# Kernel optimization log

Measured on AMD Instinct MI355X. Metric: run time of the kernel, lower is better.

## Reference

```python
import jax, jax.numpy as jnp
import numpy as np

EMBED_DIM = 512
NUM_HEADS = 8
HEAD_DIM = EMBED_DIM // NUM_HEADS


def setup_inputs() -> dict:
    key = jax.random.key(0)
    k1, k2, kw, kb, kow, kob = jax.random.split(key, 6)
    B, L, C = 2, 2048, EMBED_DIM
    s = 1.0 / np.sqrt(C)
    return {
        "x1": jax.random.normal(k1, (B, L, C), dtype=jnp.float32),
        "x2": jax.random.normal(k2, (B, L, C), dtype=jnp.float32),
        # nn.Linear(embed_dim, 3*embed_dim): weight [3C, C], bias [3C]
        "qkv_w": jax.random.uniform(kw, (3 * C, C), jnp.float32, -s, s),
        "qkv_b": jax.random.uniform(kb, (3 * C,), jnp.float32, -s, s),
        # nn.Linear(embed_dim, embed_dim): weight [C, C], bias [C]
        "out_w": jax.random.uniform(kow, (C, C), jnp.float32, -s, s),
        "out_b": jax.random.uniform(kob, (C,), jnp.float32, -s, s),
    }


def _qkv(x, qkv_w, qkv_b):
    B, L, C = x.shape
    H, D = NUM_HEADS, C // NUM_HEADS
    # Linear: x @ W^T + b, then view(B, L, H, 3, D) and split along the '3' axis
    qkv = (jnp.einsum("blc,fc->blf", x, qkv_w) + qkv_b).reshape(B, L, H, 3, D)
    qkv = jnp.transpose(qkv, (3, 0, 2, 1, 4))  # [3, B, H, L, D]
    return qkv[0], qkv[1], qkv[2]


def _attend(q, k, v):
    # q,k,v: [B, H, L, D]; scale by 1/sqrt(D)
    scale = 1.0 / np.sqrt(q.shape[-1]).astype(np.float32)
    scores = jnp.einsum("bhqd,bhkd->bhqk", q, k) * scale  # [B,H,L,L]
    attn = jax.nn.softmax(scores, axis=-1)
    out = jnp.einsum("bhqk,bhkd->bhqd", attn, v)
    B, H, L, D = out.shape
    return jnp.transpose(out, (0, 2, 1, 3)).reshape(B, L, H * D)


def reference(x1, x2, qkv_w, qkv_b, out_w, out_b):
    q1, k1, v1 = _qkv(x1, qkv_w, qkv_b)
    q2, k2, v2 = _qkv(x2, qkv_w, qkv_b)
    out1 = _attend(q1, k2, v2)  # q from x1, k/v from x2
    out2 = _attend(q2, k1, v1)  # q from x2, k/v from x1
    out1 = jnp.einsum("blc,fc->blf", out1, out_w) + out_b
    out2 = jnp.einsum("blc,fc->blf", out2, out_w) + out_b
    return (out1, out2)
```

## Files before the change

### kernel.cpp

```cpp
#include <hip/hip_runtime.h>
#include <stdint.h>

typedef unsigned short u16;
typedef unsigned int u32;
typedef short bf16x8 __attribute__((ext_vector_type(8)));
typedef float f32x4 __attribute__((ext_vector_type(4)));
typedef float f32x16 __attribute__((ext_vector_type(16)));

#define K_DIM 512

__device__ __forceinline__ u16 f2bf(float f) {
  union { float f; u32 u; } v; v.f = f;
  return (u16)((v.u + 0x8000u) >> 16);
}
__device__ __forceinline__ u32 pk2(float lo, float hi) {
  union { float f; u32 u; } a, b; a.f = lo; b.f = hi;
  return __builtin_amdgcn_perm(b.u + 0x8000u, a.u + 0x8000u, 0x07060302u);
}

__global__ void cvt_kernel(const float* __restrict__ x1, const float* __restrict__ x2,
                           const float* __restrict__ qkvw, const float* __restrict__ outw,
                           u16* __restrict__ xb, u16* __restrict__ wqkv, u16* __restrict__ wout) {
  int tid = blockIdx.x * 256 + threadIdx.x;
  const float4* src; u16* dst; int idx = tid;
  if (idx < 524288)        { src = (const float4*)x1;   dst = xb; }
  else if (idx < 1048576)  { src = (const float4*)x2;   dst = xb + 2097152; idx -= 524288; }
  else if (idx < 1245184)  { src = (const float4*)qkvw; dst = wqkv;         idx -= 1048576; }
  else                     { src = (const float4*)outw; dst = wout;         idx -= 1245184; }
  float4 v = src[idx];
  *(uint2*)&dst[idx * 4] = make_uint2(pk2(v.x, v.y), pk2(v.z, v.w));
}

#define LDA 40

__global__ __launch_bounds__(256, 3) void qkv_gemm(
    const u16* __restrict__ A, const u16* __restrict__ W, const float* __restrict__ bias,
    u16* __restrict__ qb, u16* __restrict__ kb, u16* __restrict__ vtb) {
  __shared__ __align__(16) u16 As[2][128 * LDA];
  __shared__ __align__(16) u16 Bs[2][128 * LDA];
  const int t = threadIdx.x;
  const int m0 = blockIdx.x * 128, n0 = blockIdx.y * 128;
  const int lane = t & 63, l16 = lane & 15, quad = lane >> 4;
  const int w = t >> 6;
  const int wm = (w >> 1) * 64, wn = (w & 1) * 64;
  const int sr = t >> 2, sc = (t & 3) * 8;

  const u16* Ap = A + (size_t)(m0 + sr) * K_DIM + sc;
  const u16* Wp = W + (size_t)(n0 + sr) * K_DIM + sc;

  f32x4 acc[4][4];
#pragma unroll
  for (int i = 0; i < 4; ++i)
#pragma unroll
    for (int j = 0; j < 4; ++j) acc[i][j] = (f32x4){0.f, 0.f, 0.f, 0.f};

  uint4 ra0 = *(const uint4*)(Ap);
  uint4 ra1 = *(const uint4*)(Ap + 64 * K_DIM);
  uint4 rb0 = *(const uint4*)(Wp);
  uint4 rb1 = *(const uint4*)(Wp + 64 * K_DIM);
  *(uint4*)&As[0][sr * LDA + sc] = ra0;
  *(uint4*)&As[0][(sr + 64) * LDA + sc] = ra1;
  *(uint4*)&Bs[0][sr * LDA + sc] = rb0;
  *(uint4*)&Bs[0][(sr + 64) * LDA + sc] = rb1;
  ra0 = *(const uint4*)(Ap + 32);
  ra1 = *(const uint4*)(Ap + 64 * K_DIM + 32);
  rb0 = *(const uint4*)(Wp + 32);
  rb1 = *(const uint4*)(Wp + 64 * K_DIM + 32);
  __syncthreads();

  for (int kt = 0; kt < 16; ++kt) {
    const int cur = kt & 1, nxt = cur ^ 1;
    if (kt < 15) {
      *(uint4*)&As[nxt][sr * LDA + sc] = ra0;
      *(uint4*)&As[nxt][(sr + 64) * LDA + sc] = ra1;
      *(uint4*)&Bs[nxt][sr * LDA + sc] = rb0;
      *(uint4*)&Bs[nxt][(sr + 64) * LDA + sc] = rb1;
    }
    if (kt < 14) {
      int ko = (kt + 2) * 32;
      ra0 = *(const uint4*)(Ap + ko);
      ra1 = *(const uint4*)(Ap + 64 * K_DIM + ko);
      rb0 = *(const uint4*)(Wp + ko);
      rb1 = *(const uint4*)(Wp + 64 * K_DIM + ko);
    }
    bf16x8 af[4], bfr[4];
#pragma unroll
    for (int mi = 0; mi < 4; ++mi)
      af[mi] = *(const bf16x8*)&As[cur][(wm + mi * 16 + l16) * LDA + quad * 8];
#pragma unroll
    for (int ni = 0; ni < 4; ++ni)
      bfr[ni] = *(const bf16x8*)&Bs[cur][(wn + ni * 16 + l16) * LDA + quad * 8];
#pragma unroll
    for (int mi = 0; mi < 4; ++mi)
#pragma unroll
      for (int ni = 0; ni < 4; ++ni)
        acc[mi][ni] = __builtin_amdgcn_mfma_f32_16x16x32_bf16(bfr[ni], af[mi], acc[mi][ni], 0, 0, 0);
    __syncthreads();
  }

  const int fbase = n0 + wn;
  const int h = fbase / 192;
  const int s = (fbase - h * 192) >> 6;
  float4 bv[4];
#pragma unroll
  for (int ni = 0; ni < 4; ++ni)
    bv[ni] = *(const float4*)&bias[fbase + ni * 16 + quad * 4];
  const int bh = m0 >> 11;
  const int lbase = (m0 & 2047) + wm;

  if (s == 2) {
    u16* dst = vtb + (size_t)((bh * 8 + h) * 64) * 2048;
#pragma unroll
    for (int mi = 0; mi < 4; ++mi) {
      int l = lbase + mi * 16 + l16;
#pragma unroll
      for (int ni = 0; ni < 4; ++ni)
#pragma unroll
        for (int r = 0; r < 4; ++r)
          dst[(ni * 16 + quad * 4 + r) * 2048 + l] = f2bf(acc[mi][ni][r] + bv[ni][r]);
    }
  } else {
    u16* dst = (s == 0 ? qb : kb) + (size_t)((bh * 8 + h) * 2048) * 64;
    const float sc2 = (s == 0) ? 0.18033688011112042f : 1.0f;
#pragma unroll
    for (int mi = 0; mi < 4; ++mi) {
      int l = lbase + mi * 16 + l16;
#pragma unroll
      for (int ni = 0; ni < 4; ++ni) {
        float v0 = (acc[mi][ni][0] + bv[ni][0]) * sc2;
        float v1 = (acc[mi][ni][1] + bv[ni][1]) * sc2;
        float v2 = (acc[mi][ni][2] + bv[ni][2]) * sc2;
        float v3 = (acc[mi][ni][3] + bv[ni][3]) * sc2;
        *(uint2*)&dst[(size_t)l * 64 + ni * 16 + quad * 4] = make_uint2(pk2(v0, v1), pk2(v2, v3));
      }
    }
  }
}

#define LQ 72
#define LP 72

__global__ __launch_bounds__(256, 2) void attn_kernel(
    const u16* __restrict__ qb, const u16* __restrict__ kb, const u16* __restrict__ vtb,
    u16* __restrict__ attnb) {
  __shared__ __align__(16) u16 Ks[64 * LQ];
  __shared__ __align__(16) u16 VTs[64 * LQ];
  __shared__ __align__(16) u16 Ps[128 * LP];

  const int t = threadIdx.x;
  const int w = t >> 6, lane = t & 63, l32 = lane & 31, h2 = lane >> 5;
  const int bid = blockIdx.x;
  const int comb = bid & 31;
  const int qt = bid >> 5;
  const int h = comb & 7, bb = (comb >> 3) & 1, pair = comb >> 4;
  const int in_q = pair, in_kv = pair ^ 1;

  const u16* Qg = qb + (size_t)((in_q * 2 + bb) * 8 + h) * 2048 * 64;
  const u16* Kg = kb + (size_t)((in_kv * 2 + bb) * 8 + h) * 2048 * 64;
  const u16* Vg = vtb + (size_t)((in_kv * 2 + bb) * 8 + h) * 64 * 2048;

#pragma unroll
  for (int u = 0; u < 4; ++u) {
    int idx = u * 256 + t;
    int row = idx >> 3, seg = (idx & 7) * 8;
    *(uint4*)&Ps[row * LP + seg] = *(const uint4*)(Qg + (qt * 128 + row) * 64 + seg);
  }
  const int srow = t >> 3, sseg = (t & 7) * 8;
  uint4 rk0 = *(const uint4*)(Kg + srow * 64 + sseg);
  uint4 rk1 = *(const uint4*)(Kg + (srow + 32) * 64 + sseg);
  uint4 rv0 = *(const uint4*)(Vg + srow * 2048 + sseg);
  uint4 rv1 = *(const uint4*)(Vg + (srow + 32) * 2048 + sseg);
  __syncthreads();

  bf16x8 qf[4];
#pragma unroll
  for (int ks = 0; ks < 4; ++ks)
    qf[ks] = *(const bf16x8*)&Ps[(w * 32 + l32) * LP + ks * 16 + h2 * 8];

  f32x16 oacc[2];
#pragma unroll
  for (int mi = 0; mi < 2; ++mi)
#pragma unroll
    for (int r = 0; r < 16; ++r) oacc[mi][r] = 0.f;
  float rs = 0.f;

  u16* Pw = &Ps[w * 32 * LP];

  for (int kt = 0; kt < 32; ++kt) {
    *(uint4*)&Ks[srow * LQ + sseg] = rk0;
    *(uint4*)&Ks[(srow + 32) * LQ + sseg] = rk1;
    *(uint4*)&VTs[srow * LQ + sseg] = rv0;
    *(uint4*)&VTs[(srow + 32) * LQ + sseg] = rv1;
    __syncthreads();
    if (kt < 31) {
      int ko = (kt + 1) * 64;
      rk0 = *(const uint4*)(Kg + (ko + srow) * 64 + sseg);
      rk1 = *(const uint4*)(Kg + (ko + srow + 32) * 64 + sseg);
      rv0 = *(const uint4*)(Vg + srow * 2048 + ko + sseg);
      rv1 = *(const uint4*)(Vg + (srow + 32) * 2048 + ko + sseg);
    }

    f32x16 sacc[2];
#pragma unroll
    for (int mi = 0; mi < 2; ++mi)
#pragma unroll
      for (int r = 0; r < 16; ++r) sacc[mi][r] = 0.f;
#pragma unroll
    for (int ks = 0; ks < 4; ++ks) {
      bf16x8 kfr0 = *(const bf16x8*)&Ks[(l32) * LQ + ks * 16 + h2 * 8];
      bf16x8 kfr1 = *(const bf16x8*)&Ks[(32 + l32) * LQ + ks * 16 + h2 * 8];
      sacc[0] = __builtin_amdgcn_mfma_f32_32x32x16_bf16(kfr0, qf[ks], sacc[0], 0, 0, 0);
      sacc[1] = __builtin_amdgcn_mfma_f32_32x32x16_bf16(kfr1, qf[ks], sacc[1], 0, 0, 0);
    }

#pragma unroll
    for (int mi = 0; mi < 2; ++mi)
#pragma unroll
      for (int rg = 0; rg < 4; ++rg) {
        float p0 = __builtin_amdgcn_exp2f(sacc[mi][rg * 4 + 0]);
        float p1 = __builtin_amdgcn_exp2f(sacc[mi][rg * 4 + 1]);
        float p2 = __builtin_amdgcn_exp2f(sacc[mi][rg * 4 + 2]);
        float p3 = __builtin_amdgcn_exp2f(sacc[mi][rg * 4 + 3]);
        rs += (p0 + p1) + (p2 + p3);
        *(uint2*)&Pw[l32 * LP + mi * 32 + rg * 8 + h2 * 4] = make_uint2(pk2(p0, p1), pk2(p2, p3));
      }

#pragma unroll
    for (int ks = 0; ks < 4; ++ks) {
      bf16x8 pf = *(const bf16x8*)&Pw[l32 * LP + ks * 16 + h2 * 8];
      bf16x8 vf0 = *(const bf16x8*)&VTs[(l32) * LQ + ks * 16 + h2 * 8];
      bf16x8 vf1 = *(const bf16x8*)&VTs[(32 + l32) * LQ + ks * 16 + h2 * 8];
      oacc[0] = __builtin_amdgcn_mfma_f32_32x32x16_bf16(vf0, pf, oacc[0], 0, 0, 0);
      oacc[1] = __builtin_amdgcn_mfma_f32_32x32x16_bf16(vf1, pf, oacc[1], 0, 0, 0);
    }
    __syncthreads();
  }

  rs += __shfl_xor(rs, 32);
  const float inv = 1.0f / rs;
  const int row = in_q * 4096 + bb * 2048 + qt * 128 + w * 32 + l32;
#pragma unroll
  for (int mi = 0; mi < 2; ++mi)
#pragma unroll
    for (int rg = 0; rg < 4; ++rg) {
      float v0 = oacc[mi][rg * 4 + 0] * inv;
      float v1 = oacc[mi][rg * 4 + 1] * inv;
      float v2 = oacc[mi][rg * 4 + 2] * inv;
      float v3 = oacc[mi][rg * 4 + 3] * inv;
      *(uint2*)&attnb[(size_t)row * 512 + h * 64 + mi * 32 + rg * 8 + h2 * 4] =
          make_uint2(pk2(v0, v1), pk2(v2, v3));
    }
}

__global__ __launch_bounds__(256, 2) void out_gemm(
    const u16* __restrict__ A, const u16* __restrict__ W, const float* __restrict__ bias,
    float* __restrict__ out) {
  __shared__ __align__(16) u16 As[2][64 * LDA];
  __shared__ __align__(16) u16 Bs[2][128 * LDA];
  const int t = threadIdx.x;
  const int m0 = blockIdx.x * 64, n0 = blockIdx.y * 128;
  const int lane = t & 63, l16 = lane & 15, quad = lane >> 4;
  const int w = t >> 6;
  const int wm = (w & 1) * 32, wn = (w >> 1) * 64;
  const int ar = t >> 2, ac = (t & 3) * 8;
  const int sr = t >> 2, sc = (t & 3) * 8;

  const u16* Ap = A + (size_t)(m0 + ar) * K_DIM + ac;
  const u16* Wp = W + (size_t)(n0 + sr) * K_DIM + sc;

  f32x4 acc[2][4];
#pragma unroll
  for (int i = 0; i < 2; ++i)
#pragma unroll
    for (int j = 0; j < 4; ++j) acc[i][j] = (f32x4){0.f, 0.f, 0.f, 0.f};

  uint4 ra = *(const uint4*)Ap;
  uint4 rb0 = *(const uint4*)(Wp);
  uint4 rb1 = *(const uint4*)(Wp + 64 * K_DIM);
  *(uint4*)&As[0][ar * LDA + ac] = ra;
  *(uint4*)&Bs[0][sr * LDA + sc] = rb0;
  *(uint4*)&Bs[0][(sr + 64) * LDA + sc] = rb1;
  ra = *(const uint4*)(Ap + 32);
  rb0 = *(const uint4*)(Wp + 32);
  rb1 = *(const uint4*)(Wp + 64 * K_DIM + 32);
  __syncthreads();

  for (int kt = 0; kt < 16; ++kt) {
    const int cur = kt & 1, nxt = cur ^ 1;
    if (kt < 15) {
      *(uint4*)&As[nxt][ar * LDA + ac] = ra;
      *(uint4*)&Bs[nxt][sr * LDA + sc] = rb0;
      *(uint4*)&Bs[nxt][(sr + 64) * LDA + sc] = rb1;
    }
    if (kt < 14) {
      int ko = (kt + 2) * 32;
      ra = *(const uint4*)(Ap + ko);
      rb0 = *(const uint4*)(Wp + ko);
      rb1 = *(const uint4*)(Wp + 64 * K_DIM + ko);
    }
    bf16x8 af[2], bfr[4];
#pragma unroll
    for (int mi = 0; mi < 2; ++mi)
      af[mi] = *(const bf16x8*)&As[cur][(wm + mi * 16 + l16) * LDA + quad * 8];
#pragma unroll
    for (int ni = 0; ni < 4; ++ni)
      bfr[ni] = *(const bf16x8*)&Bs[cur][(wn + ni * 16 + l16) * LDA + quad * 8];
#pragma unroll
    for (int mi = 0; mi < 2; ++mi)
#pragma unroll
      for (int ni = 0; ni < 4; ++ni)
        acc[mi][ni] = __builtin_amdgcn_mfma_f32_16x16x32_bf16(af[mi], bfr[ni], acc[mi][ni], 0, 0, 0);
    __syncthreads();
  }

#pragma unroll
  for (int ni = 0; ni < 4; ++ni) {
    int f = n0 + wn + ni * 16 + l16;
    float bv = bias[f];
#pragma unroll
    for (int mi = 0; mi < 2; ++mi)
#pragma unroll
      for (int r = 0; r < 4; ++r) {
        int m = m0 + wm + mi * 16 + quad * 4 + r;
        out[(size_t)m * 512 + f] = acc[mi][ni][r] + bv;
      }
  }
}

extern "C" void kernel_launch(void* const* d_in, const int* in_sizes, int n_in,
                              void* d_out, int out_size, void* d_ws, size_t ws_size,
                              hipStream_t stream) {
  const float* x1   = (const float*)d_in[0];
  const float* x2   = (const float*)d_in[1];
  const float* qkvw = (const float*)d_in[2];
  const float* qkvb = (const float*)d_in[3];
  const float* outw = (const float*)d_in[4];
  const float* outb = (const float*)d_in[5];
  float* out = (float*)d_out;
  char* ws = (char*)d_ws;

  u16* xb    = (u16*)(ws + 0);
  u16* wqkv  = (u16*)(ws + 8388608);
  u16* wout  = (u16*)(ws + 9961472);
  u16* qb    = (u16*)(ws + 10485760);
  u16* kb    = (u16*)(ws + 18874368);
  u16* vtb   = (u16*)(ws + 27262976);
  u16* attnb = (u16*)(ws + 0);

  cvt_kernel<<<5120, 256, 0, stream>>>(x1, x2, qkvw, outw, xb, wqkv, wout);

  dim3 g1(64, 12);
  qkv_gemm<<<g1, 256, 0, stream>>>(xb, wqkv, qkvb, qb, kb, vtb);

  attn_kernel<<<512, 256, 0, stream>>>(qb, kb, vtb, attnb);

  dim3 g3(128, 4);
  out_gemm<<<g3, 256, 0, stream>>>(attnb, wout, outb, out);
}
```

Measured before the change: 160.5 us.

## Double-buffer K/V tiles and keep P in registers via permlane32 swap

```diff
diff --git a/kernel.cpp b/kernel.cpp
--- a/kernel.cpp
+++ b/kernel.cpp
@@ -138,14 +138,12 @@
 }
 
 #define LQ 72
-#define LP 72
 
 __global__ __launch_bounds__(256, 2) void attn_kernel(
     const u16* __restrict__ qb, const u16* __restrict__ kb, const u16* __restrict__ vtb,
     u16* __restrict__ attnb) {
-  __shared__ __align__(16) u16 Ks[64 * LQ];
-  __shared__ __align__(16) u16 VTs[64 * LQ];
-  __shared__ __align__(16) u16 Ps[128 * LP];
+  __shared__ __align__(16) u16 Ks[2][64 * LQ];
+  __shared__ __align__(16) u16 VTs[2][64 * LQ];
 
   const int t = threadIdx.x;
   const int w = t >> 6, lane = t & 63, l32 = lane & 31, h2 = lane >> 5;
@@ -159,23 +157,26 @@
   const u16* Kg = kb + (size_t)((in_kv * 2 + bb) * 8 + h) * 2048 * 64;
   const u16* Vg = vtb + (size_t)((in_kv * 2 + bb) * 8 + h) * 64 * 2048;
 
-#pragma unroll
-  for (int u = 0; u < 4; ++u) {
-    int idx = u * 256 + t;
-    int row = idx >> 3, seg = (idx & 7) * 8;
-    *(uint4*)&Ps[row * LP + seg] = *(const uint4*)(Qg + (qt * 128 + row) * 64 + seg);
-  }
   const int srow = t >> 3, sseg = (t & 7) * 8;
   uint4 rk0 = *(const uint4*)(Kg + srow * 64 + sseg);
   uint4 rk1 = *(const uint4*)(Kg + (srow + 32) * 64 + sseg);
   uint4 rv0 = *(const uint4*)(Vg + srow * 2048 + sseg);
   uint4 rv1 = *(const uint4*)(Vg + (srow + 32) * 2048 + sseg);
+
+  bf16x8 qf[4];
+#pragma unroll
+  for (int ks = 0; ks < 4; ++ks)
+    qf[ks] = *(const bf16x8*)(Qg + (qt * 128 + w * 32 + l32) * 64 + ks * 16 + h2 * 8);
+
+  *(uint4*)&Ks[0][srow * LQ + sseg] = rk0;
+  *(uint4*)&Ks[0][(srow + 32) * LQ + sseg] = rk1;
+  *(uint4*)&VTs[0][srow * LQ + sseg] = rv0;
+  *(uint4*)&VTs[0][(srow + 32) * LQ + sseg] = rv1;
+  rk0 = *(const uint4*)(Kg + (64 + srow) * 64 + sseg);
+  rk1 = *(const uint4*)(Kg + (64 + srow + 32) * 64 + sseg);
+  rv0 = *(const uint4*)(Vg + srow * 2048 + 64 + sseg);
+  rv1 = *(const uint4*)(Vg + (srow + 32) * 2048 + 64 + sseg);
   __syncthreads();
-
-  bf16x8 qf[4];
-#pragma unroll
-  for (int ks = 0; ks < 4; ++ks)
-    qf[ks] = *(const bf16x8*)&Ps[(w * 32 + l32) * LP + ks * 16 + h2 * 8];
 
   f32x16 oacc[2];
 #pragma unroll
@@ -184,21 +185,9 @@
     for (int r = 0; r < 16; ++r) oacc[mi][r] = 0.f;
   float rs = 0.f;
 
-  u16* Pw = &Ps[w * 32 * LP];
-
+#pragma unroll 2
   for (int kt = 0; kt < 32; ++kt) {
-    *(uint4*)&Ks[srow * LQ + sseg] = rk0;
-    *(uint4*)&Ks[(srow + 32) * LQ + sseg] = rk1;
-    *(uint4*)&VTs[srow * LQ + sseg] = rv0;
-    *(uint4*)&VTs[(srow + 32) * LQ + sseg] = rv1;
-    __syncthreads();
-    if (kt < 31) {
-      int ko = (kt + 1) * 64;
-      rk0 = *(const uint4*)(Kg + (ko + srow) * 64 + sseg);
-      rk1 = *(const uint4*)(Kg + (ko + srow + 32) * 64 + sseg);
-      rv0 = *(const uint4*)(Vg + srow * 2048 + ko + sseg);
-      rv1 = *(const uint4*)(Vg + (srow + 32) * 2048 + ko + sseg);
-    }
+    const int cur = kt & 1, nxt = cur ^ 1;
 
     f32x16 sacc[2];
 #pragma unroll
@@ -207,33 +196,57 @@
       for (int r = 0; r < 16; ++r) sacc[mi][r] = 0.f;
 #pragma unroll
     for (int ks = 0; ks < 4; ++ks) {
-      bf16x8 kfr0 = *(const bf16x8*)&Ks[(l32) * LQ + ks * 16 + h2 * 8];
-      bf16x8 kfr1 = *(const bf16x8*)&Ks[(32 + l32) * LQ + ks * 16 + h2 * 8];
+      bf16x8 kfr0 = *(const bf16x8*)&Ks[cur][l32 * LQ + ks * 16 + h2 * 8];
+      bf16x8 kfr1 = *(const bf16x8*)&Ks[cur][(32 + l32) * LQ + ks * 16 + h2 * 8];
       sacc[0] = __builtin_amdgcn_mfma_f32_32x32x16_bf16(kfr0, qf[ks], sacc[0], 0, 0, 0);
       sacc[1] = __builtin_amdgcn_mfma_f32_32x32x16_bf16(kfr1, qf[ks], sacc[1], 0, 0, 0);
     }
 
-#pragma unroll
-    for (int mi = 0; mi < 2; ++mi)
-#pragma unroll
-      for (int rg = 0; rg < 4; ++rg) {
-        float p0 = __builtin_amdgcn_exp2f(sacc[mi][rg * 4 + 0]);
-        float p1 = __builtin_amdgcn_exp2f(sacc[mi][rg * 4 + 1]);
-        float p2 = __builtin_amdgcn_exp2f(sacc[mi][rg * 4 + 2]);
-        float p3 = __builtin_amdgcn_exp2f(sacc[mi][rg * 4 + 3]);
-        rs += (p0 + p1) + (p2 + p3);
-        *(uint2*)&Pw[l32 * LP + mi * 32 + rg * 8 + h2 * 4] = make_uint2(pk2(p0, p1), pk2(p2, p3));
+    bf16x8 pf[4];
+#pragma unroll
+    for (int mi = 0; mi < 2; ++mi) {
+      float p[16];
+#pragma unroll
+      for (int r = 0; r < 16; ++r) p[r] = __builtin_amdgcn_exp2f(sacc[mi][r]);
+#pragma unroll
+      for (int r = 0; r < 16; r += 4) rs += (p[r] + p[r + 1]) + (p[r + 2] + p[r + 3]);
+      u32 a0 = pk2(p[0], p[1]),   b0 = pk2(p[2], p[3]);
+      u32 c0 = pk2(p[4], p[5]),   d0 = pk2(p[6], p[7]);
+      u32 a1 = pk2(p[8], p[9]),   b1 = pk2(p[10], p[11]);
+      u32 c1 = pk2(p[12], p[13]), d1 = pk2(p[14], p[15]);
+      asm("v_permlane32_swap_b32 %0, %1" : "+v"(a0), "+v"(c0));
+      asm("v_permlane32_swap_b32 %0, %1" : "+v"(b0), "+v"(d0));
+      asm("v_permlane32_swap_b32 %0, %1" : "+v"(a1), "+v"(c1));
+      asm("v_permlane32_swap_b32 %0, %1" : "+v"(b1), "+v"(d1));
+      union { u32 u[4]; bf16x8 v; } f0, f1;
+      f0.u[0] = a0; f0.u[1] = b0; f0.u[2] = c0; f0.u[3] = d0;
+      f1.u[0] = a1; f1.u[1] = b1; f1.u[2] = c1; f1.u[3] = d1;
+      pf[mi * 2] = f0.v;
+      pf[mi * 2 + 1] = f1.v;
+    }
+
+    if (kt < 31) {
+      *(uint4*)&Ks[nxt][srow * LQ + sseg] = rk0;
+      *(uint4*)&Ks[nxt][(srow + 32) * LQ + sseg] = rk1;
+      *(uint4*)&VTs[nxt][srow * LQ + sseg] = rv0;
+      *(uint4*)&VTs[nxt][(srow + 32) * LQ + sseg] = rv1;
+      if (kt < 30) {
+        const int ko = (kt + 2) * 64;
+        rk0 = *(const uint4*)(Kg + (ko + srow) * 64 + sseg);
+        rk1 = *(const uint4*)(Kg + (ko + srow + 32) * 64 + sseg);
+        rv0 = *(const uint4*)(Vg + srow * 2048 + ko + sseg);
+        rv1 = *(const uint4*)(Vg + (srow + 32) * 2048 + ko + sseg);
       }
+    }
 
 #pragma unroll
     for (int ks = 0; ks < 4; ++ks) {
-      bf16x8 pf = *(const bf16x8*)&Pw[l32 * LP + ks * 16 + h2 * 8];
-      bf16x8 vf0 = *(const bf16x8*)&VTs[(l32) * LQ + ks * 16 + h2 * 8];
-      bf16x8 vf1 = *(const bf16x8*)&VTs[(32 + l32) * LQ + ks * 16 + h2 * 8];
-      oacc[0] = __builtin_amdgcn_mfma_f32_32x32x16_bf16(vf0, pf, oacc[0], 0, 0, 0);
-      oacc[1] = __builtin_amdgcn_mfma_f32_32x32x16_bf16(vf1, pf, oacc[1], 0, 0, 0);
-    }
-    __syncthreads();
+      bf16x8 vf0 = *(const bf16x8*)&VTs[cur][l32 * LQ + ks * 16 + h2 * 8];
+      bf16x8 vf1 = *(const bf16x8*)&VTs[cur][(32 + l32) * LQ + ks * 16 + h2 * 8];
+      oacc[0] = __builtin_amdgcn_mfma_f32_32x32x16_bf16(vf0, pf[ks], oacc[0], 0, 0, 0);
+      oacc[1] = __builtin_amdgcn_mfma_f32_32x32x16_bf16(vf1, pf[ks], oacc[1], 0, 0, 0);
+    }
+    if (kt < 31) __syncthreads();
   }
 
   rs += __shfl_xor(rs, 32);
```

Measured after the change: 154.1 us. 4.0% less time.

## Software-pipeline attention loop and keep P in registers via permlane swap

Applied to the files above, without the earlier changes.

```diff
diff --git a/kernel.cpp b/kernel.cpp
--- a/kernel.cpp
+++ b/kernel.cpp
@@ -138,14 +138,56 @@
 }
 
 #define LQ 72
-#define LP 72
+
+#define SPHASE(SS, KBUF)                                                          \
+  do {                                                                            \
+    _Pragma("unroll") for (int r_ = 0; r_ < 16; ++r_) {                           \
+      SS[0][r_] = 0.f; SS[1][r_] = 0.f;                                           \
+    }                                                                             \
+    _Pragma("unroll") for (int ks_ = 0; ks_ < 4; ++ks_) {                         \
+      bf16x8 kfr0 = *(const bf16x8*)&Ks[KBUF][l32 * LQ + ks_ * 16 + h2 * 8];      \
+      bf16x8 kfr1 = *(const bf16x8*)&Ks[KBUF][(32 + l32) * LQ + ks_ * 16 + h2 * 8]; \
+      SS[0] = __builtin_amdgcn_mfma_f32_32x32x16_bf16(kfr0, qf[ks_], SS[0], 0, 0, 0); \
+      SS[1] = __builtin_amdgcn_mfma_f32_32x32x16_bf16(kfr1, qf[ks_], SS[1], 0, 0, 0); \
+    }                                                                             \
+  } while (0)
+
+#define SOFTPV(SS, VBUF)                                                          \
+  do {                                                                            \
+    bf16x8 pf[4];                                                                 \
+    _Pragma("unroll") for (int mi_ = 0; mi_ < 2; ++mi_) {                         \
+      float p[16];                                                                \
+      _Pragma("unroll") for (int r_ = 0; r_ < 16; ++r_)                           \
+        p[r_] = __builtin_amdgcn_exp2f(SS[mi_][r_]);                              \
+      _Pragma("unroll") for (int r_ = 0; r_ < 16; r_ += 4)                        \
+        rs += (p[r_] + p[r_ + 1]) + (p[r_ + 2] + p[r_ + 3]);                      \
+      u32 a0 = pk2(p[0], p[1]),   b0 = pk2(p[2], p[3]);                           \
+      u32 c0 = pk2(p[4], p[5]),   d0 = pk2(p[6], p[7]);                           \
+      u32 a1 = pk2(p[8], p[9]),   b1 = pk2(p[10], p[11]);                         \
+      u32 c1 = pk2(p[12], p[13]), d1 = pk2(p[14], p[15]);                         \
+      asm("v_permlane32_swap_b32 %0, %1" : "+v"(a0), "+v"(c0));                   \
+      asm("v_permlane32_swap_b32 %0, %1" : "+v"(b0), "+v"(d0));                   \
+      asm("v_permlane32_swap_b32 %0, %1" : "+v"(a1), "+v"(c1));                   \
+      asm("v_permlane32_swap_b32 %0, %1" : "+v"(b1), "+v"(d1));                   \
+      union { u32 u[4]; bf16x8 v; } f0_, f1_;                                     \
+      f0_.u[0] = a0; f0_.u[1] = b0; f0_.u[2] = c0; f0_.u[3] = d0;                 \
+      f1_.u[0] = a1; f1_.u[1] = b1; f1_.u[2] = c1; f1_.u[3] = d1;                 \
+      pf[mi_ * 2] = f0_.v; pf[mi_ * 2 + 1] = f1_.v;                               \
+    }                                                                             \
+    const u16* vb_ = (const u16*)VTs + (VBUF) * (64 * LQ);                        \
+    _Pragma("unroll") for (int ks_ = 0; ks_ < 4; ++ks_) {                         \
+      bf16x8 vf0 = *(const bf16x8*)&vb_[l32 * LQ + ks_ * 16 + h2 * 8];            \
+      bf16x8 vf1 = *(const bf16x8*)&vb_[(32 + l32) * LQ + ks_ * 16 + h2 * 8];     \
+      oacc[0] = __builtin_amdgcn_mfma_f32_32x32x16_bf16(vf0, pf[ks_], oacc[0], 0, 0, 0); \
+      oacc[1] = __builtin_amdgcn_mfma_f32_32x32x16_bf16(vf1, pf[ks_], oacc[1], 0, 0, 0); \
+    }                                                                             \
+  } while (0)
 
 __global__ __launch_bounds__(256, 2) void attn_kernel(
     const u16* __restrict__ qb, const u16* __restrict__ kb, const u16* __restrict__ vtb,
     u16* __restrict__ attnb) {
-  __shared__ __align__(16) u16 Ks[64 * LQ];
-  __shared__ __align__(16) u16 VTs[64 * LQ];
-  __shared__ __align__(16) u16 Ps[128 * LP];
+  __shared__ __align__(16) u16 Ks[2][64 * LQ];
+  __shared__ __align__(16) u16 VTs[4][64 * LQ];
 
   const int t = threadIdx.x;
   const int w = t >> 6, lane = t & 63, l32 = lane & 31, h2 = lane >> 5;
@@ -159,23 +201,30 @@
   const u16* Kg = kb + (size_t)((in_kv * 2 + bb) * 8 + h) * 2048 * 64;
   const u16* Vg = vtb + (size_t)((in_kv * 2 + bb) * 8 + h) * 64 * 2048;
 
-#pragma unroll
-  for (int u = 0; u < 4; ++u) {
-    int idx = u * 256 + t;
-    int row = idx >> 3, seg = (idx & 7) * 8;
-    *(uint4*)&Ps[row * LP + seg] = *(const uint4*)(Qg + (qt * 128 + row) * 64 + seg);
-  }
   const int srow = t >> 3, sseg = (t & 7) * 8;
   uint4 rk0 = *(const uint4*)(Kg + srow * 64 + sseg);
   uint4 rk1 = *(const uint4*)(Kg + (srow + 32) * 64 + sseg);
   uint4 rv0 = *(const uint4*)(Vg + srow * 2048 + sseg);
   uint4 rv1 = *(const uint4*)(Vg + (srow + 32) * 2048 + sseg);
-  __syncthreads();
 
   bf16x8 qf[4];
 #pragma unroll
   for (int ks = 0; ks < 4; ++ks)
-    qf[ks] = *(const bf16x8*)&Ps[(w * 32 + l32) * LP + ks * 16 + h2 * 8];
+    qf[ks] = *(const bf16x8*)(Qg + (qt * 128 + w * 32 + l32) * 64 + ks * 16 + h2 * 8);
+
+  auto stage = [&](int kbuf, int vbuf) {
+    *(uint4*)&Ks[kbuf][srow * LQ + sseg] = rk0;
+    *(uint4*)&Ks[kbuf][(srow + 32) * LQ + sseg] = rk1;
+    *(uint4*)&VTs[vbuf][srow * LQ + sseg] = rv0;
+    *(uint4*)&VTs[vbuf][(srow + 32) * LQ + sseg] = rv1;
+  };
+  auto gload = [&](int kt) {
+    const int ko = kt * 64;
+    rk0 = *(const uint4*)(Kg + (ko + srow) * 64 + sseg);
+    rk1 = *(const uint4*)(Kg + (ko + srow + 32) * 64 + sseg);
+    rv0 = *(const uint4*)(Vg + srow * 2048 + ko + sseg);
+    rv1 = *(const uint4*)(Vg + (srow + 32) * 2048 + ko + sseg);
+  };
 
   f32x16 oacc[2];
 #pragma unroll
@@ -183,58 +232,33 @@
 #pragma unroll
     for (int r = 0; r < 16; ++r) oacc[mi][r] = 0.f;
   float rs = 0.f;
-
-  u16* Pw = &Ps[w * 32 * LP];
-
-  for (int kt = 0; kt < 32; ++kt) {
-    *(uint4*)&Ks[srow * LQ + sseg] = rk0;
-    *(uint4*)&Ks[(srow + 32) * LQ + sseg] = rk1;
-    *(uint4*)&VTs[srow * LQ + sseg] = rv0;
-    *(uint4*)&VTs[(srow + 32) * LQ + sseg] = rv1;
+  f32x16 sA[2], sB[2];
+
+  stage(0, 0);
+  gload(1);
+  __syncthreads();
+
+  SPHASE(sA, 0);
+  stage(1, 1);
+  gload(2);
+  __syncthreads();
+
+#pragma unroll 1
+  for (int it = 0; it < 16; ++it) {
+    const int e = (it & 1) << 1;
+    SPHASE(sB, 1);
+    SOFTPV(sA, e);
+    if (it == 15) break;
+    stage(0, e ^ 2);
+    gload(2 * it + 3);
     __syncthreads();
-    if (kt < 31) {
-      int ko = (kt + 1) * 64;
-      rk0 = *(const uint4*)(Kg + (ko + srow) * 64 + sseg);
-      rk1 = *(const uint4*)(Kg + (ko + srow + 32) * 64 + sseg);
-      rv0 = *(const uint4*)(Vg + srow * 2048 + ko + sseg);
-      rv1 = *(const uint4*)(Vg + (srow + 32) * 2048 + ko + sseg);
-    }
-
-    f32x16 sacc[2];
-#pragma unroll
-    for (int mi = 0; mi < 2; ++mi)
-#pragma unroll
-      for (int r = 0; r < 16; ++r) sacc[mi][r] = 0.f;
-#pragma unroll
-    for (int ks = 0; ks < 4; ++ks) {
-      bf16x8 kfr0 = *(const bf16x8*)&Ks[(l32) * LQ + ks * 16 + h2 * 8];
-      bf16x8 kfr1 = *(const bf16x8*)&Ks[(32 + l32) * LQ + ks * 16 + h2 * 8];
-      sacc[0] = __builtin_amdgcn_mfma_f32_32x32x16_bf16(kfr0, qf[ks], sacc[0], 0, 0, 0);
-      sacc[1] = __builtin_amdgcn_mfma_f32_32x32x16_bf16(kfr1, qf[ks], sacc[1], 0, 0, 0);
-    }
-
-#pragma unroll
-    for (int mi = 0; mi < 2; ++mi)
-#pragma unroll
-      for (int rg = 0; rg < 4; ++rg) {
-        float p0 = __builtin_amdgcn_exp2f(sacc[mi][rg * 4 + 0]);
-        float p1 = __builtin_amdgcn_exp2f(sacc[mi][rg * 4 + 1]);
-        float p2 = __builtin_amdgcn_exp2f(sacc[mi][rg * 4 + 2]);
-        float p3 = __builtin_amdgcn_exp2f(sacc[mi][rg * 4 + 3]);
-        rs += (p0 + p1) + (p2 + p3);
-        *(uint2*)&Pw[l32 * LP + mi * 32 + rg * 8 + h2 * 4] = make_uint2(pk2(p0, p1), pk2(p2, p3));
-      }
-
-#pragma unroll
-    for (int ks = 0; ks < 4; ++ks) {
-      bf16x8 pf = *(const bf16x8*)&Pw[l32 * LP + ks * 16 + h2 * 8];
-      bf16x8 vf0 = *(const bf16x8*)&VTs[(l32) * LQ + ks * 16 + h2 * 8];
-      bf16x8 vf1 = *(const bf16x8*)&VTs[(32 + l32) * LQ + ks * 16 + h2 * 8];
-      oacc[0] = __builtin_amdgcn_mfma_f32_32x32x16_bf16(vf0, pf, oacc[0], 0, 0, 0);
-      oacc[1] = __builtin_amdgcn_mfma_f32_32x32x16_bf16(vf1, pf, oacc[1], 0, 0, 0);
-    }
+    SPHASE(sA, 0);
+    SOFTPV(sB, e + 1);
+    stage(1, e ^ 3);
+    if (it < 14) gload(2 * it + 4);
     __syncthreads();
   }
+  SOFTPV(sB, 3);
 
   rs += __shfl_xor(rs, 32);
   const float inv = 1.0f / rs;
```

After: 150.5 us. -6.2%, faster.

## Keep softmax probabilities in registers and double-buffer 128-key tiles in attention

Applied to the files above, without the earlier changes.

```diff
diff --git a/kernel.cpp b/kernel.cpp
--- a/kernel.cpp
+++ b/kernel.cpp
@@ -138,14 +138,48 @@
 }
 
 #define LQ 72
-#define LP 72
+#define LV 136
+
+#define SOFTPK(SLO, SHI, PF)                                                      \
+  do {                                                                            \
+    float p[16];                                                                  \
+    _Pragma("unroll") for (int r_ = 0; r_ < 16; ++r_)                             \
+      p[r_] = __builtin_amdgcn_exp2f(SLO[r_]);                                    \
+    _Pragma("unroll") for (int r_ = 0; r_ < 16; r_ += 4)                          \
+      rs += (p[r_] + p[r_ + 1]) + (p[r_ + 2] + p[r_ + 3]);                        \
+    u32 a0 = pk2(p[0], p[1]),   b0 = pk2(p[2], p[3]);                             \
+    u32 c0 = pk2(p[4], p[5]),   d0 = pk2(p[6], p[7]);                             \
+    u32 a1 = pk2(p[8], p[9]),   b1 = pk2(p[10], p[11]);                           \
+    u32 c1 = pk2(p[12], p[13]), d1 = pk2(p[14], p[15]);                           \
+    _Pragma("unroll") for (int r_ = 0; r_ < 16; ++r_)                             \
+      p[r_] = __builtin_amdgcn_exp2f(SHI[r_]);                                    \
+    _Pragma("unroll") for (int r_ = 0; r_ < 16; r_ += 4)                          \
+      rs += (p[r_] + p[r_ + 1]) + (p[r_ + 2] + p[r_ + 3]);                        \
+    u32 a2 = pk2(p[0], p[1]),   b2 = pk2(p[2], p[3]);                             \
+    u32 c2 = pk2(p[4], p[5]),   d2 = pk2(p[6], p[7]);                             \
+    u32 a3 = pk2(p[8], p[9]),   b3 = pk2(p[10], p[11]);                           \
+    u32 c3 = pk2(p[12], p[13]), d3 = pk2(p[14], p[15]);                           \
+    asm("v_permlane32_swap_b32 %0, %1" : "+v"(a0), "+v"(c0));                     \
+    asm("v_permlane32_swap_b32 %0, %1" : "+v"(b0), "+v"(d0));                     \
+    asm("v_permlane32_swap_b32 %0, %1" : "+v"(a1), "+v"(c1));                     \
+    asm("v_permlane32_swap_b32 %0, %1" : "+v"(b1), "+v"(d1));                     \
+    asm("v_permlane32_swap_b32 %0, %1" : "+v"(a2), "+v"(c2));                     \
+    asm("v_permlane32_swap_b32 %0, %1" : "+v"(b2), "+v"(d2));                     \
+    asm("v_permlane32_swap_b32 %0, %1" : "+v"(a3), "+v"(c3));                     \
+    asm("v_permlane32_swap_b32 %0, %1" : "+v"(b3), "+v"(d3));                     \
+    union { u32 u[4]; bf16x8 v; } f0_, f1_, f2_, f3_;                             \
+    f0_.u[0] = a0; f0_.u[1] = b0; f0_.u[2] = c0; f0_.u[3] = d0;                   \
+    f1_.u[0] = a1; f1_.u[1] = b1; f1_.u[2] = c1; f1_.u[3] = d1;                   \
+    f2_.u[0] = a2; f2_.u[1] = b2; f2_.u[2] = c2; f2_.u[3] = d2;                   \
+    f3_.u[0] = a3; f3_.u[1] = b3; f3_.u[2] = c3; f3_.u[3] = d3;                   \
+    PF[0] = f0_.v; PF[1] = f1_.v; PF[2] = f2_.v; PF[3] = f3_.v;                   \
+  } while (0)
 
 __global__ __launch_bounds__(256, 2) void attn_kernel(
     const u16* __restrict__ qb, const u16* __restrict__ kb, const u16* __restrict__ vtb,
     u16* __restrict__ attnb) {
-  __shared__ __align__(16) u16 Ks[64 * LQ];
-  __shared__ __align__(16) u16 VTs[64 * LQ];
-  __shared__ __align__(16) u16 Ps[128 * LP];
+  __shared__ __align__(16) u16 Ks[2][128 * LQ];
+  __shared__ __align__(16) u16 VTs[2][64 * LV];
 
   const int t = threadIdx.x;
   const int w = t >> 6, lane = t & 63, l32 = lane & 31, h2 = lane >> 5;
@@ -159,23 +193,31 @@
   const u16* Kg = kb + (size_t)((in_kv * 2 + bb) * 8 + h) * 2048 * 64;
   const u16* Vg = vtb + (size_t)((in_kv * 2 + bb) * 8 + h) * 64 * 2048;
 
-#pragma unroll
-  for (int u = 0; u < 4; ++u) {
-    int idx = u * 256 + t;
-    int row = idx >> 3, seg = (idx & 7) * 8;
-    *(uint4*)&Ps[row * LP + seg] = *(const uint4*)(Qg + (qt * 128 + row) * 64 + seg);
-  }
   const int srow = t >> 3, sseg = (t & 7) * 8;
-  uint4 rk0 = *(const uint4*)(Kg + srow * 64 + sseg);
-  uint4 rk1 = *(const uint4*)(Kg + (srow + 32) * 64 + sseg);
-  uint4 rv0 = *(const uint4*)(Vg + srow * 2048 + sseg);
-  uint4 rv1 = *(const uint4*)(Vg + (srow + 32) * 2048 + sseg);
-  __syncthreads();
+  const int vrow = t >> 4, vcol = (t & 15) * 8;
+  uint4 rk[4], rv[4];
+
+  auto gload = [&](int kt) {
+#pragma unroll
+    for (int i = 0; i < 4; ++i)
+      rk[i] = *(const uint4*)(Kg + (kt * 128 + srow + i * 32) * 64 + sseg);
+#pragma unroll
+    for (int i = 0; i < 4; ++i)
+      rv[i] = *(const uint4*)(Vg + (vrow + i * 16) * 2048 + kt * 128 + vcol);
+  };
+  auto stage = [&](int buf) {
+#pragma unroll
+    for (int i = 0; i < 4; ++i)
+      *(uint4*)&Ks[buf][(srow + i * 32) * LQ + sseg] = rk[i];
+#pragma unroll
+    for (int i = 0; i < 4; ++i)
+      *(uint4*)&VTs[buf][(vrow + i * 16) * LV + vcol] = rv[i];
+  };
 
   bf16x8 qf[4];
 #pragma unroll
   for (int ks = 0; ks < 4; ++ks)
-    qf[ks] = *(const bf16x8*)&Ps[(w * 32 + l32) * LP + ks * 16 + h2 * 8];
+    qf[ks] = *(const bf16x8*)(Qg + (qt * 128 + w * 32 + l32) * 64 + ks * 16 + h2 * 8);
 
   f32x16 oacc[2];
 #pragma unroll
@@ -184,56 +226,56 @@
     for (int r = 0; r < 16; ++r) oacc[mi][r] = 0.f;
   float rs = 0.f;
 
-  u16* Pw = &Ps[w * 32 * LP];
-
-  for (int kt = 0; kt < 32; ++kt) {
-    *(uint4*)&Ks[srow * LQ + sseg] = rk0;
-    *(uint4*)&Ks[(srow + 32) * LQ + sseg] = rk1;
-    *(uint4*)&VTs[srow * LQ + sseg] = rv0;
-    *(uint4*)&VTs[(srow + 32) * LQ + sseg] = rv1;
-    __syncthreads();
-    if (kt < 31) {
-      int ko = (kt + 1) * 64;
-      rk0 = *(const uint4*)(Kg + (ko + srow) * 64 + sseg);
-      rk1 = *(const uint4*)(Kg + (ko + srow + 32) * 64 + sseg);
-      rv0 = *(const uint4*)(Vg + srow * 2048 + ko + sseg);
-      rv1 = *(const uint4*)(Vg + (srow + 32) * 2048 + ko + sseg);
-    }
-
-    f32x16 sacc[2];
-#pragma unroll
-    for (int mi = 0; mi < 2; ++mi)
-#pragma unroll
-      for (int r = 0; r < 16; ++r) sacc[mi][r] = 0.f;
+  gload(0);
+  stage(0);
+  gload(1);
+  __syncthreads();
+
+#pragma unroll 2
+  for (int kt = 0; kt < 16; ++kt) {
+    const int cur = kt & 1;
+    if (kt < 15) stage(cur ^ 1);
+    if (kt < 14) gload(kt + 2);
+
+    const u16* kb_ = &Ks[cur][0];
+    const u16* vb_ = &VTs[cur][0];
+
+    f32x16 s0, s1, s2, s3;
+#pragma unroll
+    for (int r = 0; r < 16; ++r) { s0[r] = 0.f; s1[r] = 0.f; s2[r] = 0.f; s3[r] = 0.f; }
 #pragma unroll
     for (int ks = 0; ks < 4; ++ks) {
-      bf16x8 kfr0 = *(const bf16x8*)&Ks[(l32) * LQ + ks * 16 + h2 * 8];
-      bf16x8 kfr1 = *(const bf16x8*)&Ks[(32 + l32) * LQ + ks * 16 + h2 * 8];
-      sacc[0] = __builtin_amdgcn_mfma_f32_32x32x16_bf16(kfr0, qf[ks], sacc[0], 0, 0, 0);
-      sacc[1] = __builtin_amdgcn_mfma_f32_32x32x16_bf16(kfr1, qf[ks], sacc[1], 0, 0, 0);
-    }
-
-#pragma unroll
-    for (int mi = 0; mi < 2; ++mi)
-#pragma unroll
-      for (int rg = 0; rg < 4; ++rg) {
-        float p0 = __builtin_amdgcn_exp2f(sacc[mi][rg * 4 + 0]);
-        float p1 = __builtin_amdgcn_exp2f(sacc[mi][rg * 4 + 1]);
-        float p2 = __builtin_amdgcn_exp2f(sacc[mi][rg * 4 + 2]);
-        float p3 = __builtin_amdgcn_exp2f(sacc[mi][rg * 4 + 3]);
-        rs += (p0 + p1) + (p2 + p3);
-        *(uint2*)&Pw[l32 * LP + mi * 32 + rg * 8 + h2 * 4] = make_uint2(pk2(p0, p1), pk2(p2, p3));
-      }
-
+      bf16x8 a0 = *(const bf16x8*)&kb_[(l32) * LQ + ks * 16 + h2 * 8];
+      bf16x8 a1 = *(const bf16x8*)&kb_[(32 + l32) * LQ + ks * 16 + h2 * 8];
+      s0 = __builtin_amdgcn_mfma_f32_32x32x16_bf16(a0, qf[ks], s0, 0, 0, 0);
+      s1 = __builtin_amdgcn_mfma_f32_32x32x16_bf16(a1, qf[ks], s1, 0, 0, 0);
+    }
 #pragma unroll
     for (int ks = 0; ks < 4; ++ks) {
-      bf16x8 pf = *(const bf16x8*)&Pw[l32 * LP + ks * 16 + h2 * 8];
-      bf16x8 vf0 = *(const bf16x8*)&VTs[(l32) * LQ + ks * 16 + h2 * 8];
-      bf16x8 vf1 = *(const bf16x8*)&VTs[(32 + l32) * LQ + ks * 16 + h2 * 8];
-      oacc[0] = __builtin_amdgcn_mfma_f32_32x32x16_bf16(vf0, pf, oacc[0], 0, 0, 0);
-      oacc[1] = __builtin_amdgcn_mfma_f32_32x32x16_bf16(vf1, pf, oacc[1], 0, 0, 0);
-    }
-    __syncthreads();
+      bf16x8 a2 = *(const bf16x8*)&kb_[(64 + l32) * LQ + ks * 16 + h2 * 8];
+      bf16x8 a3 = *(const bf16x8*)&kb_[(96 + l32) * LQ + ks * 16 + h2 * 8];
+      s2 = __builtin_amdgcn_mfma_f32_32x32x16_bf16(a2, qf[ks], s2, 0, 0, 0);
+      s3 = __builtin_amdgcn_mfma_f32_32x32x16_bf16(a3, qf[ks], s3, 0, 0, 0);
+    }
+
+    bf16x8 pf[4];
+    SOFTPK(s0, s1, pf);
+#pragma unroll
+    for (int ks = 0; ks < 4; ++ks) {
+      bf16x8 v0 = *(const bf16x8*)&vb_[(l32) * LV + ks * 16 + h2 * 8];
+      bf16x8 v1 = *(const bf16x8*)&vb_[(32 + l32) * LV + ks * 16 + h2 * 8];
+      oacc[0] = __builtin_amdgcn_mfma_f32_32x32x16_bf16(v0, pf[ks], oacc[0], 0, 0, 0);
+      oacc[1] = __builtin_amdgcn_mfma_f32_32x32x16_bf16(v1, pf[ks], oacc[1], 0, 0, 0);
+    }
+    SOFTPK(s2, s3, pf);
+#pragma unroll
+    for (int ks = 0; ks < 4; ++ks) {
+      bf16x8 v0 = *(const bf16x8*)&vb_[(l32) * LV + 64 + ks * 16 + h2 * 8];
+      bf16x8 v1 = *(const bf16x8*)&vb_[(32 + l32) * LV + 64 + ks * 16 + h2 * 8];
+      oacc[0] = __builtin_amdgcn_mfma_f32_32x32x16_bf16(v0, pf[ks], oacc[0], 0, 0, 0);
+      oacc[1] = __builtin_amdgcn_mfma_f32_32x32x16_bf16(v1, pf[ks], oacc[1], 0, 0, 0);
+    }
+    if (kt < 15) __syncthreads();
   }
 
   rs += __shfl_xor(rs, 32);
```

New measurement: 196.3 us. 1.22x slower.
